# Optimization experiments

Measured on AMD Instinct MI355X. Metric: run time of the kernel, lower is better.

The kernel has to match this reference:

```python
import jax, jax.numpy as jnp
import numpy as np

WS = 8          # window_size
HEADS = 4       # num_heads
C = 64          # channels
D_K = C // HEADS


def window_partition(x, ws):
    # x: [B, C, H, W] -> [B*nH*nW, ws*ws, C]
    B, Cc, H, W = x.shape
    x = x.reshape(B, Cc, H // ws, ws, W // ws, ws)
    x = jnp.transpose(x, (0, 2, 4, 3, 5, 1))
    return x.reshape(-1, ws * ws, Cc)


def window_reverse(x, H, W, ws):
    # x: [B*nH*nW, ws*ws, C] -> [B, C, H, W]
    B = x.shape[0] // ((H // ws) * (W // ws))
    x = x.reshape(B, H // ws, W // ws, ws, ws, -1)
    x = jnp.transpose(x, (0, 5, 1, 3, 2, 4))
    return x.reshape(B, -1, H, W)


def setup_inputs() -> dict:
    key = jax.random.key(0)
    ks = jax.random.split(key, 9)
    s = 1.0 / np.sqrt(C)
    return {
        "x":  jax.random.normal(ks[0], (4, C, 512, 512), dtype=jnp.float32),
        "wq": jax.random.normal(ks[1], (C, C), dtype=jnp.float32) * s,
        "bq": jax.random.normal(ks[2], (C,), dtype=jnp.float32) * 0.01,
        "wk": jax.random.normal(ks[3], (C, C), dtype=jnp.float32) * s,
        "bk": jax.random.normal(ks[4], (C,), dtype=jnp.float32) * 0.01,
        "wv": jax.random.normal(ks[5], (C, C), dtype=jnp.float32) * s,
        "bv": jax.random.normal(ks[6], (C,), dtype=jnp.float32) * 0.01,
        "wp": jax.random.normal(ks[7], (C, C), dtype=jnp.float32) * s,
        "bp": jax.random.normal(ks[8], (C,), dtype=jnp.float32) * 0.01,
    }


def reference(x, wq, bq, wk, bk, wv, bv, wp, bp):
    B, Cc, H, W = x.shape
    ws2 = WS * WS
    xw = window_partition(x, WS)                      # [nWin, ws2, C]
    # 1x1 conv == per-token linear on channel dim
    q = jnp.einsum('ntc,oc->nto', xw, wq) + bq
    k = jnp.einsum('ntc,oc->nto', xw, wk) + bk
    v = jnp.einsum('ntc,oc->nto', xw, wv) + bv
    # Faithful to the original (non-standard) reshape into heads
    q = q.reshape(-1, HEADS, ws2, D_K)
    k = k.reshape(-1, HEADS, ws2, D_K)
    v = v.reshape(-1, HEADS, ws2, D_K)
    scale = 1.0 / np.sqrt(D_K).astype(np.float32)
    attn = jnp.einsum('nhtd,nhsd->nhts', q, k) * scale  # [nWin, H, ws2, ws2]
    attn = jax.nn.softmax(attn, axis=-1)               # dropout omitted (eval)
    out = jnp.einsum('nhts,nhsd->nhtd', attn, v)
    out = out.reshape(-1, ws2, Cc)
    y = window_reverse(out, H, W, WS)                  # [B, C, H, W]
    y = jnp.einsum('bchw,oc->bohw', y, wp) + bp[None, :, None, None]
    return y
```

## Files before the change

kernel.cpp:

```cpp
#include <hip/hip_runtime.h>

typedef unsigned short u16;
typedef unsigned int   u32;
typedef float f32x4  __attribute__((ext_vector_type(4)));
typedef short bf16x8 __attribute__((ext_vector_type(8)));

#define CCH  64
#define HH   512
#define WWD  512
#define WS_  8
#define NWIN 16384

__device__ __align__(16) unsigned char g_wprep[32768 + 1024];

__device__ __forceinline__ u16 f2bf(float f) {
    union { float f; u32 u; } v; v.f = f;
    u32 r = v.u + 0x7fffu + ((v.u >> 16) & 1u);
    return (u16)(r >> 16);
}
__device__ __forceinline__ u32 pack2(float a, float b) {
    return (u32)f2bf(a) | ((u32)f2bf(b) << 16);
}

__device__ __forceinline__ u32 swz8(u32 t) { return (t ^ (t >> 3)) & 7u; }
__device__ __forceinline__ u32 sx_off(u32 t, u32 c) {
    return ((t << 7) + (c << 1)) ^ (swz8(t) << 4);
}
__device__ __forceinline__ u32 qk_off(u32 elem) {
    u32 t = elem >> 6;
    return (elem << 1) ^ (swz8(t) << 4);
}
__device__ __forceinline__ u32 vt_off(u32 h, u32 d, u32 s2) {
    return ((h << 11) + (d << 7) + (s2 << 1)) ^ (swz8(d) << 4);
}
__device__ __forceinline__ u32 p_off(u32 s, u32 s2) {
    return ((s << 7) + (s2 << 1)) ^ (swz8(s) << 4);
}
__device__ __forceinline__ u32 x2_off(u32 w, u32 tr, u32 c) {
    u32 base = 8192u + ((tr >> 3) << 13) + (w << 11);
    u32 b = ((tr & 7) << 8) + (c << 2);
    return base + (b ^ (swz8(tr) << 5));
}

__global__ void wmsa_prep(const float* wq, const float* wk, const float* wv, const float* wp,
                          const float* bq, const float* bk, const float* bv, const float* bp)
{
    int tid = threadIdx.x;
    #pragma unroll
    for (int q = 0; q < 8; ++q) {
        int cid = q * 256 + tid;
        int l  = cid & 63;
        int kk = (cid >> 6) & 1;
        int to = (cid >> 7) & 3;
        int m  = (cid >> 9) & 3;
        const float* wm = (m == 0) ? wq : (m == 1) ? wk : (m == 2) ? wv : wp;
        int o  = 16 * to + (l & 15);
        int c0 = kk * 32 + (l >> 4) * 8;
        const float4* src = (const float4*)(wm + o * 64 + c0);
        float4 a = src[0], b2 = src[1];
        uint4 pk = { pack2(a.x, a.y), pack2(a.z, a.w), pack2(b2.x, b2.y), pack2(b2.z, b2.w) };
        *(uint4*)(g_wprep + (size_t)cid * 16) = pk;
    }
    const float* bsrc = (tid < 64) ? bq : (tid < 128) ? bk : (tid < 192) ? bv : bp;
    ((float*)(g_wprep + 32768))[tid] = bsrc[tid & 63];
}

__global__ __launch_bounds__(256, 2) void wmsa_kernel(
    const float* __restrict__ x, float* __restrict__ y)
{
    __shared__ __align__(16) unsigned char smem[65536];

    const int tid  = threadIdx.x;
    const int lane = tid & 63;
    const int w    = tid >> 6;
    const int lg   = lane >> 4;
    const int lr   = lane & 15;

    const int bid = blockIdx.x;
    const int win = ((bid & 7) << 11) | (bid >> 3);
    const int b   = win >> 12;
    const int wh  = (win >> 6) & 63;
    const int wwi = win & 63;

    const float* __restrict__ gb = (const float*)(g_wprep + 32768);
    const f32x4 zf = {0.f, 0.f, 0.f, 0.f};

    #pragma unroll
    for (int it = 0; it < 2; ++it) {
        int e = it * 256 + tid;
        int c = e >> 3;
        int i = e & 7;
        const float4* src = (const float4*)(x +
            ((((size_t)b * CCH + c) * HH + wh * WS_ + i) * WWD + wwi * WS_));
        float4 v0 = src[0], v1 = src[1];
        u16 pk[8] = { f2bf(v0.x), f2bf(v0.y), f2bf(v0.z), f2bf(v0.w),
                      f2bf(v1.x), f2bf(v1.y), f2bf(v1.z), f2bf(v1.w) };
        #pragma unroll
        for (int j = 0; j < 8; ++j) {
            int t = i * 8 + j;
            *(u16*)(smem + sx_off((u32)t, (u32)c)) = pk[j];
        }
    }
    __syncthreads();

    bf16x8 ax0, ax1;
    {
        int tA = w * 16 + lr;
        ax0 = *(const bf16x8*)(smem + sx_off((u32)tA, (u32)(lg * 8)));
        ax1 = *(const bf16x8*)(smem + sx_off((u32)tA, (u32)(32 + lg * 8)));
    }

    #pragma unroll
    for (int m = 0; m < 2; ++m) {
        u32 rbase = 8192u + (u32)m * 8192u;
        #pragma unroll
        for (int to = 0; to < 4; ++to) {
            bf16x8 b0 = *(const bf16x8*)(g_wprep + ((((m * 4 + to) * 2 + 0) * 64 + lane) << 4));
            bf16x8 b1 = *(const bf16x8*)(g_wprep + ((((m * 4 + to) * 2 + 1) * 64 + lane) << 4));
            f32x4 acc = __builtin_amdgcn_mfma_f32_16x16x32_bf16(ax0, b0, zf, 0, 0, 0);
            acc = __builtin_amdgcn_mfma_f32_16x16x32_bf16(ax1, b1, acc, 0, 0, 0);
            float bias = gb[m * 64 + to * 16 + lr];
            #pragma unroll
            for (int r = 0; r < 4; ++r) {
                int t = w * 16 + lg * 4 + r;
                int o = to * 16 + lr;
                *(u16*)(smem + rbase + qk_off((u32)(t * 64 + o))) = f2bf(acc[r] + bias);
            }
        }
    }

    {
        f32x4 av[4]; float bv4[4];
        #pragma unroll
        for (int to = 0; to < 4; ++to) {
            bf16x8 b0 = *(const bf16x8*)(g_wprep + ((((2 * 4 + to) * 2 + 0) * 64 + lane) << 4));
            bf16x8 b1 = *(const bf16x8*)(g_wprep + ((((2 * 4 + to) * 2 + 1) * 64 + lane) << 4));
            f32x4 acc = __builtin_amdgcn_mfma_f32_16x16x32_bf16(ax0, b0, zf, 0, 0, 0);
            acc = __builtin_amdgcn_mfma_f32_16x16x32_bf16(ax1, b1, acc, 0, 0, 0);
            av[to] = acc;
            bv4[to] = gb[128 + to * 16 + lr];
        }
        #pragma unroll
        for (int r = 0; r < 4; ++r) {
            uint2 u;
            u.x = pack2(av[0][r] + bv4[0], av[1][r] + bv4[1]);
            u.y = pack2(av[2][r] + bv4[2], av[3][r] + bv4[3]);
            *(uint2*)(smem + 24576u + vt_off((u32)w, (u32)lr, (u32)(lg * 16 + r * 4))) = u;
        }
    }

    bf16x8 kz = {0, 0, 0, 0, 0, 0, 0, 0};
    bf16x8 kf[4], qf[4];
    const bool gact = (lg < 2);
    #pragma unroll
    for (int tt = 0; tt < 4; ++tt) {
        int srow = tt * 16 + lr;
        kf[tt] = kz; qf[tt] = kz;
        if (gact) {
            u32 e = (u32)(w * 1024 + srow * 16 + lg * 8);
            qf[tt] = *(const bf16x8*)(smem + 8192u  + qk_off(e));
            kf[tt] = *(const bf16x8*)(smem + 16384u + qk_off(e));
        }
    }
    f32x4 sacc[4][4];
    #pragma unroll
    for (int t2 = 0; t2 < 4; ++t2)
        #pragma unroll
        for (int t1 = 0; t1 < 4; ++t1)
            sacc[t2][t1] = __builtin_amdgcn_mfma_f32_16x16x32_bf16(kf[t2], qf[t1], zf, 0, 0, 0);

    const float ksc = 0.25f * 1.44269504088896341f;
    const u32 pslab = 32768u + (u32)w * 8192u;
    #pragma unroll
    for (int t1 = 0; t1 < 4; ++t1) {
        float mx = -3.4e38f;
        #pragma unroll
        for (int t2 = 0; t2 < 4; ++t2)
            #pragma unroll
            for (int r = 0; r < 4; ++r) mx = fmaxf(mx, sacc[t2][t1][r]);
        mx = fmaxf(mx, __shfl_xor(mx, 16));
        mx = fmaxf(mx, __shfl_xor(mx, 32));
        float sum = 0.f;
        #pragma unroll
        for (int t2 = 0; t2 < 4; ++t2)
            #pragma unroll
            for (int r = 0; r < 4; ++r) {
                float e = exp2f((sacc[t2][t1][r] - mx) * ksc);
                sacc[t2][t1][r] = e;
                sum += e;
            }
        sum += __shfl_xor(sum, 16);
        sum += __shfl_xor(sum, 32);
        float inv = 1.0f / sum;
        int s = t1 * 16 + lr;
        #pragma unroll
        for (int t2 = 0; t2 < 4; ++t2) {
            uint2 u;
            u.x = pack2(sacc[t2][t1][0] * inv, sacc[t2][t1][1] * inv);
            u.y = pack2(sacc[t2][t1][2] * inv, sacc[t2][t1][3] * inv);
            *(uint2*)(smem + pslab + p_off((u32)s, (u32)(t2 * 16 + lg * 4))) = u;
        }
    }

    {
        bf16x8 vf0 = *(const bf16x8*)(smem + 24576u + vt_off((u32)w, (u32)lr, (u32)(lg * 8)));
        bf16x8 vf1 = *(const bf16x8*)(smem + 24576u + vt_off((u32)w, (u32)lr, (u32)(32 + lg * 8)));
        #pragma unroll
        for (int t1 = 0; t1 < 4; ++t1) {
            bf16x8 p0 = *(const bf16x8*)(smem + pslab + p_off((u32)(t1 * 16 + lr), (u32)(lg * 8)));
            bf16x8 p1 = *(const bf16x8*)(smem + pslab + p_off((u32)(t1 * 16 + lr), (u32)(32 + lg * 8)));
            f32x4 acc = __builtin_amdgcn_mfma_f32_16x16x32_bf16(p0, vf0, zf, 0, 0, 0);
            acc = __builtin_amdgcn_mfma_f32_16x16x32_bf16(p1, vf1, acc, 0, 0, 0);
            int tr = t1 * 4 + lg;
            #pragma unroll
            for (int r = 0; r < 4; ++r)
                *(float*)(smem + x2_off((u32)w, (u32)tr, (u32)(r * 16 + lr))) = acc[r];
        }
    }

    {
        bf16x8 ao0, ao1;
        {
            const float4* xp = (const float4*)(smem + x2_off((u32)w, (u32)lr, (u32)(lg * 8)));
            float4 v0 = xp[0], v1 = xp[1];
            uint4 uu = { pack2(v0.x, v0.y), pack2(v0.z, v0.w), pack2(v1.x, v1.y), pack2(v1.z, v1.w) };
            ao0 = *(bf16x8*)&uu;
            const float4* xq = (const float4*)(smem + x2_off((u32)w, (u32)lr, (u32)(32 + lg * 8)));
            float4 v2 = xq[0], v3 = xq[1];
            uint4 vv = { pack2(v2.x, v2.y), pack2(v2.z, v2.w), pack2(v3.x, v3.y), pack2(v3.z, v3.w) };
            ao1 = *(bf16x8*)&vv;
        }
        #pragma unroll
        for (int to = 0; to < 4; ++to) {
            bf16x8 b0 = *(const bf16x8*)(g_wprep + ((((3 * 4 + to) * 2 + 0) * 64 + lane) << 4));
            bf16x8 b1 = *(const bf16x8*)(g_wprep + ((((3 * 4 + to) * 2 + 1) * 64 + lane) << 4));
            f32x4 acc = __builtin_amdgcn_mfma_f32_16x16x32_bf16(ao0, b0, zf, 0, 0, 0);
            acc = __builtin_amdgcn_mfma_f32_16x16x32_bf16(ao1, b1, acc, 0, 0, 0);
            #pragma unroll
            for (int r = 0; r < 4; ++r) {
                int o  = to * 16 + lr;
                int tq = lg * 4 + r;
                *(float*)(smem + pslab + (u32)((o * 19 + tq) << 2)) = acc[r];
            }
        }
    }
    __syncthreads();

    {
        int i = lane >> 3, j = lane & 7;
        int t = i * 8 + j;
        u32 srcslab = 32768u + (u32)(t >> 4) * 8192u;
        int tq = t & 15;
        size_t ybase = (((size_t)b * CCH * HH) + (size_t)(wh * WS_ + i)) * WWD + (size_t)(wwi * WS_ + j);
        #pragma unroll
        for (int oo = 0; oo < 16; ++oo) {
            int o = w * 16 + oo;
            float v = *(const float*)(smem + srcslab + (u32)((o * 19 + tq) << 2)) + gb[192 + o];
            y[ybase + (size_t)o * (HH * (size_t)WWD)] = v;
        }
    }
}

extern "C" void kernel_launch(void* const* d_in, const int* in_sizes, int n_in,
                              void* d_out, int out_size, void* d_ws, size_t ws_size,
                              hipStream_t stream) {
    const float* x  = (const float*)d_in[0];
    const float* wq = (const float*)d_in[1];
    const float* bq = (const float*)d_in[2];
    const float* wk = (const float*)d_in[3];
    const float* bk = (const float*)d_in[4];
    const float* wv = (const float*)d_in[5];
    const float* bv = (const float*)d_in[6];
    const float* wp = (const float*)d_in[7];
    const float* bp = (const float*)d_in[8];
    float* y = (float*)d_out;

    hipLaunchKernelGGL(wmsa_prep, dim3(1), dim3(256), 0, stream,
                       wq, wk, wv, wp, bq, bk, bv, bp);
    hipLaunchKernelGGL(wmsa_kernel, dim3(NWIN), dim3(256), 0, stream, x, y);
}
```

Before: 610.9 us.

## Keep softmax probabilities in registers and halve LDS for higher occupancy

```diff
diff --git a/kernel.cpp b/kernel.cpp
--- a/kernel.cpp
+++ b/kernel.cpp
@@ -2,8 +2,9 @@
 
 typedef unsigned short u16;
 typedef unsigned int   u32;
-typedef float f32x4  __attribute__((ext_vector_type(4)));
-typedef short bf16x8 __attribute__((ext_vector_type(8)));
+typedef float f32x4   __attribute__((ext_vector_type(4)));
+typedef short bf16x8  __attribute__((ext_vector_type(8)));
+typedef short bf16x4s __attribute__((ext_vector_type(4)));
 
 #define CCH  64
 #define HH   512
@@ -13,28 +14,39 @@
 
 __device__ __align__(16) unsigned char g_wprep[32768 + 1024];
 
-__device__ __forceinline__ u16 f2bf(float f) {
-    union { float f; u32 u; } v; v.f = f;
-    u32 r = v.u + 0x7fffu + ((v.u >> 16) & 1u);
-    return (u16)(r >> 16);
+__device__ __forceinline__ u16 f2bfh(float f) {
+    __bf16 h = (__bf16)f;
+    union { __bf16 b; u16 u; } cv; cv.b = h; return cv.u;
 }
 __device__ __forceinline__ u32 pack2(float a, float b) {
-    return (u32)f2bf(a) | ((u32)f2bf(b) << 16);
+    return (u32)f2bfh(a) | ((u32)f2bfh(b) << 16);
+}
+__device__ __forceinline__ bf16x4s mk4(float a, float b, float c, float d) {
+    bf16x4s v;
+    v[0] = (short)f2bfh(a); v[1] = (short)f2bfh(b);
+    v[2] = (short)f2bfh(c); v[3] = (short)f2bfh(d);
+    return v;
+}
+
+__device__ __forceinline__ f32x4 mfma16(bf16x4s a, bf16x4s b, f32x4 c) {
+#if __has_builtin(__builtin_amdgcn_mfma_f32_16x16x16bf16_1k)
+    return __builtin_amdgcn_mfma_f32_16x16x16bf16_1k(a, b, c, 0, 0, 0);
+#else
+    asm("v_mfma_f32_16x16x16_bf16 %0, %1, %2, %0" : "+v"(c) : "v"(a), "v"(b));
+    return c;
+#endif
 }
 
 __device__ __forceinline__ u32 swz8(u32 t) { return (t ^ (t >> 3)) & 7u; }
 __device__ __forceinline__ u32 sx_off(u32 t, u32 c) {
     return ((t << 7) + (c << 1)) ^ (swz8(t) << 4);
 }
-__device__ __forceinline__ u32 qk_off(u32 elem) {
-    u32 t = elem >> 6;
-    return (elem << 1) ^ (swz8(t) << 4);
+__device__ __forceinline__ u32 qk_off(u32 e) {
+    u32 t = e >> 6;
+    return (e << 1) ^ (((t >> 2) & 3u) << 4);
 }
 __device__ __forceinline__ u32 vt_off(u32 h, u32 d, u32 s2) {
-    return ((h << 11) + (d << 7) + (s2 << 1)) ^ (swz8(d) << 4);
-}
-__device__ __forceinline__ u32 p_off(u32 s, u32 s2) {
-    return ((s << 7) + (s2 << 1)) ^ (swz8(s) << 4);
+    return (h << 11) + (d << 7) + (((s2 << 1) ^ ((d & 15u) << 3)) & 127u);
 }
 __device__ __forceinline__ u32 x2_off(u32 w, u32 tr, u32 c) {
     u32 base = 8192u + ((tr >> 3) << 13) + (w << 11);
@@ -65,10 +77,10 @@
     ((float*)(g_wprep + 32768))[tid] = bsrc[tid & 63];
 }
 
-__global__ __launch_bounds__(256, 2) void wmsa_kernel(
+__global__ __launch_bounds__(256, 4) void wmsa_kernel(
     const float* __restrict__ x, float* __restrict__ y)
 {
-    __shared__ __align__(16) unsigned char smem[65536];
+    __shared__ __align__(16) unsigned char smem[32768];
 
     const int tid  = threadIdx.x;
     const int lane = tid & 63;
@@ -93,8 +105,8 @@
         const float4* src = (const float4*)(x +
             ((((size_t)b * CCH + c) * HH + wh * WS_ + i) * WWD + wwi * WS_));
         float4 v0 = src[0], v1 = src[1];
-        u16 pk[8] = { f2bf(v0.x), f2bf(v0.y), f2bf(v0.z), f2bf(v0.w),
-                      f2bf(v1.x), f2bf(v1.y), f2bf(v1.z), f2bf(v1.w) };
+        u16 pk[8] = { f2bfh(v0.x), f2bfh(v0.y), f2bfh(v0.z), f2bfh(v0.w),
+                      f2bfh(v1.x), f2bfh(v1.y), f2bfh(v1.z), f2bfh(v1.w) };
         #pragma unroll
         for (int j = 0; j < 8; ++j) {
             int t = i * 8 + j;
@@ -124,7 +136,7 @@
             for (int r = 0; r < 4; ++r) {
                 int t = w * 16 + lg * 4 + r;
                 int o = to * 16 + lr;
-                *(u16*)(smem + rbase + qk_off((u32)(t * 64 + o))) = f2bf(acc[r] + bias);
+                *(u16*)(smem + rbase + qk_off((u32)(t * 64 + o))) = f2bfh(acc[r] + bias);
             }
         }
     }
@@ -149,35 +161,31 @@
         }
     }
 
-    bf16x8 kz = {0, 0, 0, 0, 0, 0, 0, 0};
-    bf16x8 kf[4], qf[4];
-    const bool gact = (lg < 2);
+    bf16x4s kf4[4], qf4[4];
     #pragma unroll
     for (int tt = 0; tt < 4; ++tt) {
-        int srow = tt * 16 + lr;
-        kf[tt] = kz; qf[tt] = kz;
-        if (gact) {
-            u32 e = (u32)(w * 1024 + srow * 16 + lg * 8);
-            qf[tt] = *(const bf16x8*)(smem + 8192u  + qk_off(e));
-            kf[tt] = *(const bf16x8*)(smem + 16384u + qk_off(e));
-        }
-    }
-    f32x4 sacc[4][4];
+        u32 e = (u32)(w * 1024 + (tt * 16 + lr) * 16 + lg * 4);
+        qf4[tt] = *(const bf16x4s*)(smem + 8192u  + qk_off(e));
+        kf4[tt] = *(const bf16x4s*)(smem + 16384u + qk_off(e));
+    }
+    bf16x4s vfb[4];
     #pragma unroll
     for (int t2 = 0; t2 < 4; ++t2)
-        #pragma unroll
-        for (int t1 = 0; t1 < 4; ++t1)
-            sacc[t2][t1] = __builtin_amdgcn_mfma_f32_16x16x32_bf16(kf[t2], qf[t1], zf, 0, 0, 0);
+        vfb[t2] = *(const bf16x4s*)(smem + 24576u + vt_off((u32)w, (u32)lr, (u32)(t2 * 16 + lg * 4)));
 
     const float ksc = 0.25f * 1.44269504088896341f;
-    const u32 pslab = 32768u + (u32)w * 8192u;
     #pragma unroll
     for (int t1 = 0; t1 < 4; ++t1) {
+        f32x4 sc[4];
+        #pragma unroll
+        for (int t2 = 0; t2 < 4; ++t2)
+            sc[t2] = mfma16(kf4[t2], qf4[t1], zf);
+
         float mx = -3.4e38f;
         #pragma unroll
         for (int t2 = 0; t2 < 4; ++t2)
             #pragma unroll
-            for (int r = 0; r < 4; ++r) mx = fmaxf(mx, sacc[t2][t1][r]);
+            for (int r = 0; r < 4; ++r) mx = fmaxf(mx, sc[t2][r]);
         mx = fmaxf(mx, __shfl_xor(mx, 16));
         mx = fmaxf(mx, __shfl_xor(mx, 32));
         float sum = 0.f;
@@ -185,39 +193,27 @@
         for (int t2 = 0; t2 < 4; ++t2)
             #pragma unroll
             for (int r = 0; r < 4; ++r) {
-                float e = exp2f((sacc[t2][t1][r] - mx) * ksc);
-                sacc[t2][t1][r] = e;
-                sum += e;
+                float e = exp2f((sc[t2][r] - mx) * ksc);
+                sc[t2][r] = e; sum += e;
             }
         sum += __shfl_xor(sum, 16);
         sum += __shfl_xor(sum, 32);
         float inv = 1.0f / sum;
-        int s = t1 * 16 + lr;
+
+        f32x4 oacc = zf;
         #pragma unroll
         for (int t2 = 0; t2 < 4; ++t2) {
-            uint2 u;
-            u.x = pack2(sacc[t2][t1][0] * inv, sacc[t2][t1][1] * inv);
-            u.y = pack2(sacc[t2][t1][2] * inv, sacc[t2][t1][3] * inv);
-            *(uint2*)(smem + pslab + p_off((u32)s, (u32)(t2 * 16 + lg * 4))) = u;
-        }
-    }
-
-    {
-        bf16x8 vf0 = *(const bf16x8*)(smem + 24576u + vt_off((u32)w, (u32)lr, (u32)(lg * 8)));
-        bf16x8 vf1 = *(const bf16x8*)(smem + 24576u + vt_off((u32)w, (u32)lr, (u32)(32 + lg * 8)));
-        #pragma unroll
-        for (int t1 = 0; t1 < 4; ++t1) {
-            bf16x8 p0 = *(const bf16x8*)(smem + pslab + p_off((u32)(t1 * 16 + lr), (u32)(lg * 8)));
-            bf16x8 p1 = *(const bf16x8*)(smem + pslab + p_off((u32)(t1 * 16 + lr), (u32)(32 + lg * 8)));
-            f32x4 acc = __builtin_amdgcn_mfma_f32_16x16x32_bf16(p0, vf0, zf, 0, 0, 0);
-            acc = __builtin_amdgcn_mfma_f32_16x16x32_bf16(p1, vf1, acc, 0, 0, 0);
-            int tr = t1 * 4 + lg;
-            #pragma unroll
-            for (int r = 0; r < 4; ++r)
-                *(float*)(smem + x2_off((u32)w, (u32)tr, (u32)(r * 16 + lr))) = acc[r];
-        }
-    }
-
+            bf16x4s pf = mk4(sc[t2][0] * inv, sc[t2][1] * inv,
+                             sc[t2][2] * inv, sc[t2][3] * inv);
+            oacc = mfma16(pf, vfb[t2], oacc);
+        }
+        int tr = t1 * 4 + lg;
+        #pragma unroll
+        for (int r = 0; r < 4; ++r)
+            *(float*)(smem + x2_off((u32)w, (u32)tr, (u32)(r * 16 + lr))) = oacc[r];
+    }
+
+    f32x4 racc[4];
     {
         bf16x8 ao0, ao1;
         {
@@ -235,27 +231,28 @@
             bf16x8 b0 = *(const bf16x8*)(g_wprep + ((((3 * 4 + to) * 2 + 0) * 64 + lane) << 4));
             bf16x8 b1 = *(const bf16x8*)(g_wprep + ((((3 * 4 + to) * 2 + 1) * 64 + lane) << 4));
             f32x4 acc = __builtin_amdgcn_mfma_f32_16x16x32_bf16(ao0, b0, zf, 0, 0, 0);
-            acc = __builtin_amdgcn_mfma_f32_16x16x32_bf16(ao1, b1, acc, 0, 0, 0);
-            #pragma unroll
-            for (int r = 0; r < 4; ++r) {
-                int o  = to * 16 + lr;
-                int tq = lg * 4 + r;
-                *(float*)(smem + pslab + (u32)((o * 19 + tq) << 2)) = acc[r];
-            }
+            racc[to] = __builtin_amdgcn_mfma_f32_16x16x32_bf16(ao1, b1, acc, 0, 0, 0);
         }
     }
     __syncthreads();
 
     {
+        #pragma unroll
+        for (int to = 0; to < 4; ++to) {
+            u32 word = (u32)w * 1032u + (u32)((to * 16 + lr) * 16 + lg * 4);
+            *(f32x4*)(smem + (word << 2)) = racc[to];
+        }
+    }
+    __syncthreads();
+
+    {
         int i = lane >> 3, j = lane & 7;
-        int t = i * 8 + j;
-        u32 srcslab = 32768u + (u32)(t >> 4) * 8192u;
-        int tq = t & 15;
+        u32 base = (u32)(lane >> 4) * 1032u + (u32)(lane & 15);
         size_t ybase = (((size_t)b * CCH * HH) + (size_t)(wh * WS_ + i)) * WWD + (size_t)(wwi * WS_ + j);
         #pragma unroll
         for (int oo = 0; oo < 16; ++oo) {
             int o = w * 16 + oo;
-            float v = *(const float*)(smem + srcslab + (u32)((o * 19 + tq) << 2)) + gb[192 + o];
+            float v = ((const float*)smem)[base + ((u32)o << 4)] + gb[192 + o];
             y[ybase + (size_t)o * (HH * (size_t)WWD)] = v;
         }
     }
```

Result: faster. 560.1 us (-8.3%).
